# Kernel optimization log

Hardware: AMD Instinct MI355X
Metric: run time of the kernel (lower is better)

Reference implementation:

```python
import jax, jax.numpy as jnp
import numpy as np

N, E, G, P = 65536, 1048576, 512, 128   # nodes, edges, graphs, nodes per graph
K = 64                                   # sort-pool k (fixed in module)
NUM_CLASSES = 10
FEAT = 128


def _gcn_conv(x, W, b, src, dst):
    # PyG GCNConv: linear, add self-loops, symmetric-normalized aggregation, bias
    h = x @ W
    deg = jnp.ones((N,), x.dtype).at[dst].add(1.0)       # self-loop + in-degree
    dinv = jax.lax.rsqrt(deg)
    coef = (dinv[src] * dinv[dst])[:, None]
    agg = jax.ops.segment_sum(h[src] * coef, dst, num_segments=N)
    agg = agg + h * (dinv * dinv)[:, None]               # self-loop messages
    return agg + b


def setup_inputs() -> dict:
    key = jax.random.key(0)
    ks = jax.random.split(key, 12)
    x = jax.random.normal(ks[0], (N, FEAT), jnp.float32)
    src = jax.random.randint(ks[1], (E,), 0, N, dtype=jnp.int32)
    off = jax.random.randint(ks[2], (E,), 0, P, dtype=jnp.int32)
    dst = (src // P) * P + off                           # keep edges intra-graph
    edge_index = jnp.stack([src, dst])
    # balanced batch vector (implicit): node n belongs to graph n // P
    def lin(k, i, o):
        return jax.random.normal(k, (i, o), jnp.float32) / np.float32(np.sqrt(i))
    return {
        "x": x,
        "W1": lin(ks[3], FEAT, 128), "b1": jnp.zeros((128,), jnp.float32),
        "W2": lin(ks[4], 128, 64),   "b2": jnp.zeros((64,), jnp.float32),
        "W3": lin(ks[5], 64, 32),    "b3": jnp.zeros((32,), jnp.float32),
        "W4": lin(ks[6], 32, 32),    "b4": jnp.zeros((32,), jnp.float32),
        "W5": lin(ks[7], 256, 16).T, "b5": jnp.zeros((16,), jnp.float32),   # Conv1d(1,16,256,256)
        "W6": jax.random.normal(ks[8], (32, 16, 5), jnp.float32) * 0.1,      # Conv1d(16,32,5) OIH
        "b6": jnp.zeros((32,), jnp.float32),
        "Wf1": lin(ks[9], 896, 128), "bf1": jnp.zeros((128,), jnp.float32),
        "Wf2": lin(ks[10], 128, NUM_CLASSES), "bf2": jnp.zeros((NUM_CLASSES,), jnp.float32),
        "edge_index": edge_index,
    }


def reference(x, W1, b1, W2, b2, W3, b3, W4, b4, W5, b5, W6, b6,
              Wf1, bf1, Wf2, bf2, edge_index):
    src, dst = edge_index[0], edge_index[1]
    x1 = jnp.tanh(_gcn_conv(x, W1, b1, src, dst))
    x2 = jnp.tanh(_gcn_conv(x1, W2, b2, src, dst))
    x3 = jnp.tanh(_gcn_conv(x2, W3, b3, src, dst))
    x4 = jnp.tanh(_gcn_conv(x3, W4, b4, src, dst))
    h = jnp.concatenate([x1, x2, x3, x4], axis=-1)       # [N, 256]
    C = h.shape[-1]
    # global_sort_pool: balanced graphs of P nodes -> sort desc by last channel, take top-K
    hg = h.reshape(G, P, C)
    order = jnp.argsort(-hg[:, :, -1], axis=1)[:, :K]    # [G, K]
    pooled = jnp.take_along_axis(hg, order[:, :, None], axis=1)   # [G, K, C]
    # Conv1d(1, 16, 256, stride=256): kernel == stride == C, so per-node matmul
    z = jnp.einsum('gtj,cj->gct', pooled, W5) + b5[None, :, None]  # [G,16,64]
    z = jax.nn.relu(z)
    z = z.reshape(G, 16, -1, 2).max(axis=-1)                       # MaxPool1d(2,2) -> [G,16,32]
    z = jax.lax.conv_general_dilated(z, W6, (1,), 'VALID',
                                     dimension_numbers=('NCH', 'OIH', 'NCH'))
    z = jax.nn.relu(z + b6[None, :, None])                          # [G,32,28]
    z = z.reshape(G, -1)                                            # [G,896]
    out = jax.nn.relu(z @ Wf1 + bf1)
    # dropout is identity at eval time
    return jax.nn.log_softmax(out @ Wf2 + bf2, axis=-1)
```

## Files before the change

kernel.cpp:

```cpp
#include <hip/hip_runtime.h>

#define N_EDGES 1048576
#define N_GRAPH 512
#define MAXE    2560
#define CHUNK   2048
#define SBLK    (N_EDGES / CHUNK)

typedef __attribute__((ext_vector_type(4))) float floatx4;
typedef __attribute__((ext_vector_type(2))) float floatx2;
typedef __attribute__((ext_vector_type(4))) int intx4;

__global__ void scatter_kernel(const int* __restrict__ src, const int* __restrict__ dst,
                               unsigned* __restrict__ cstab, unsigned short* __restrict__ ebuf) {
    __shared__ unsigned short sbuf[CHUNK];
    __shared__ unsigned short sg[CHUNK];
    __shared__ unsigned lhist[512];
    __shared__ unsigned lscan[512];
    const int t = threadIdx.x;
    const int b = blockIdx.x;
    lhist[t] = 0; lhist[t + 256] = 0;
    __syncthreads();
    const intx4* s4 = (const intx4*)(src + b * CHUNK) + t * 2;
    const intx4* d4 = (const intx4*)(dst + b * CHUNK) + t * 2;
    unsigned short gg[8], pk[8], rr[8];
#pragma unroll
    for (int h = 0; h < 2; ++h) {
        intx4 sv = s4[h], dv = d4[h];
        int ss[4] = {sv.x, sv.y, sv.z, sv.w};
        int dd[4] = {dv.x, dv.y, dv.z, dv.w};
#pragma unroll
        for (int j = 0; j < 4; ++j) {
            unsigned g = ((unsigned)dd[j]) >> 7;
            gg[h * 4 + j] = (unsigned short)g;
            pk[h * 4 + j] = (unsigned short)((ss[j] & 127) | ((dd[j] & 127) << 8));
            rr[h * 4 + j] = (unsigned short)atomicAdd(&lhist[g], 1u);
        }
    }
    __syncthreads();
    unsigned a0 = lhist[t], a1 = lhist[t + 256];
    lscan[t] = a0; lscan[t + 256] = a1;
    __syncthreads();
    for (int d = 1; d < 512; d <<= 1) {
        unsigned v0 = (t >= d) ? lscan[t - d] : 0u;
        unsigned v1 = (t + 256 >= d) ? lscan[t + 256 - d] : 0u;
        __syncthreads();
        lscan[t] += v0; lscan[t + 256] += v1;
        __syncthreads();
    }
    lscan[t] -= a0; lscan[t + 256] -= a1;
    cstab[(size_t)t * SBLK + b]         = (a0 << 16) | lscan[t];
    cstab[(size_t)(t + 256) * SBLK + b] = (a1 << 16) | lscan[t + 256];
    __syncthreads();
#pragma unroll
    for (int j = 0; j < 8; ++j) {
        unsigned pos = lscan[gg[j]] + rr[j];
        sbuf[pos] = pk[j]; sg[pos] = gg[j];
    }
    __syncthreads();
    for (int i = t; i < CHUNK; i += 256)
        ebuf[(size_t)b * CHUNK + i] = sbuf[i];
    (void)sg;
}

template<int CIN, int COUT>
__device__ void gcn_layer(const float* Xin, float* Xio,
                          const float* __restrict__ W, const float* __restrict__ Bv,
                          const float* __restrict__ dinv, const int* __restrict__ offs,
                          const float* __restrict__ epack, int tid)
{
    constexpr int CL  = COUT / 4;
    constexpr int NPT = 128 / (1024 / CL);
    const int grp = tid / CL, cl = tid % CL;

    float acc[NPT][4];
#pragma unroll
    for (int ni = 0; ni < NPT; ++ni)
#pragma unroll
        for (int j = 0; j < 4; ++j) acc[ni][j] = 0.f;

    for (int k = 0; k < CIN; k += 4) {
        floatx4 xv[NPT];
#pragma unroll
        for (int ni = 0; ni < NPT; ++ni)
            xv[ni] = *(const floatx4*)(Xin + (grp * NPT + ni) * CIN + k);
#pragma unroll
        for (int i = 0; i < 4; ++i) {
            floatx4 wv = *(const floatx4*)(W + (k + i) * COUT + cl * 4);
#pragma unroll
            for (int ni = 0; ni < NPT; ++ni)
#pragma unroll
                for (int j = 0; j < 4; ++j)
                    acc[ni][j] += xv[ni][i] * wv[j];
        }
    }
    __syncthreads();
#pragma unroll
    for (int ni = 0; ni < NPT; ++ni) {
        floatx4 v; v[0] = acc[ni][0]; v[1] = acc[ni][1]; v[2] = acc[ni][2]; v[3] = acc[ni][3];
        *(floatx4*)(Xio + (grp * NPT + ni) * COUT + cl * 4) = v;
    }
    __syncthreads();

    floatx4 bv = *(const floatx4*)(Bv + cl * 4);
    float vout[NPT][4];
#pragma unroll
    for (int ni = 0; ni < NPT; ++ni) {
        int n = grp * NPT + ni;
        float a[4] = {0.f, 0.f, 0.f, 0.f};
        int o0 = offs[n], o1 = offs[n + 1];
        for (int p = o0; p < o1; ++p) {
            floatx2 e = *(const floatx2*)(epack + 2 * p);
            float cf = e[0];
            int s = (int)__float_as_uint(e[1]);
            floatx4 h = *(const floatx4*)(Xio + s * COUT + cl * 4);
#pragma unroll
            for (int j = 0; j < 4; ++j) a[j] += h[j] * cf;
        }
        float dn = dinv[n], dnn = dn * dn;
#pragma unroll
        for (int j = 0; j < 4; ++j)
            vout[ni][j] = tanhf(a[j] + acc[ni][j] * dnn + bv[j]);
    }
    __syncthreads();
#pragma unroll
    for (int ni = 0; ni < NPT; ++ni) {
        floatx4 v; v[0] = vout[ni][0]; v[1] = vout[ni][1]; v[2] = vout[ni][2]; v[3] = vout[ni][3];
        *(floatx4*)(Xio + (grp * NPT + ni) * COUT + cl * 4) = v;
    }
    __syncthreads();
}

__global__ __launch_bounds__(1024, 1) void mega_kernel(
    const float* __restrict__ x,
    const float* __restrict__ W1, const float* __restrict__ b1,
    const float* __restrict__ W2, const float* __restrict__ b2,
    const float* __restrict__ W3, const float* __restrict__ b3,
    const float* __restrict__ W4, const float* __restrict__ b4,
    const float* __restrict__ W5, const float* __restrict__ b5,
    const float* __restrict__ W6, const float* __restrict__ b6,
    const float* __restrict__ Wf1, const float* __restrict__ bf1,
    const float* __restrict__ Wf2, const float* __restrict__ bf2,
    const unsigned* __restrict__ cstab, const unsigned short* __restrict__ ebuf,
    float* __restrict__ out)
{
    __shared__ __align__(16) char pool[162048];
    int*   ldeg = (int*)(pool + 0);
    int*   offs = (int*)(pool + 512);
    float* dinv = (float*)(pool + 1040);
    float* key  = (float*)(pool + 1552);
    unsigned short* ord = (unsigned short*)(pool + 2064);
    float* epack = (float*)(pool + 2304);
    float* W5s   = (float*)(pool + 2304);
    float* X1   = (float*)(pool + 22784);
    float* X2   = (float*)(pool + 88320);
    float* X3   = (float*)(pool + 121088);
    float* X4   = (float*)(pool + 137472);
    float* SCR  = (float*)(pool + 153856);
    float* Zs   = SCR;
    float* ZMP  = SCR + 1024;
    float* Z896 = SCR;
    float* PART = SCR + 1024;
    float* FC1  = SCR + 896;
    float* LG   = SCR;

    const int g   = blockIdx.x;
    const int tid = threadIdx.x;

    int myc = 0;
    unsigned short ev[24];
    if (tid < SBLK) {
        unsigned cs = cstab[(size_t)g * SBLK + tid];
        int start = (int)(cs & 0xFFFFu);
        myc = (int)(cs >> 16);
        if (myc > 24) myc = 24;
        const unsigned short* run = ebuf + (size_t)tid * CHUNK + start;
#pragma unroll
        for (int w = 0; w < 24; ++w)
            ev[w] = (w < myc) ? run[w] : (unsigned short)0;
    }

    if (tid < 128) ldeg[tid] = 0;
    __syncthreads();
#pragma unroll
    for (int w = 0; w < 24; ++w)
        if (w < myc) atomicAdd(&ldeg[(ev[w] >> 8) & 127], 1);
    __syncthreads();
    if (tid < 64) {
        int v0 = ldeg[2 * tid], v1 = ldeg[2 * tid + 1];
        int s = v0 + v1;
        for (int d = 1; d < 64; d <<= 1) {
            int u = __shfl_up(s, d, 64);
            if (tid >= d) s += u;
        }
        int e1 = s - v1, e2 = s;
        offs[2 * tid + 1] = (e1 < MAXE) ? e1 : MAXE;
        offs[2 * tid + 2] = (e2 < MAXE) ? e2 : MAXE;
        if (tid == 0) offs[0] = 0;
    }
    if (tid >= 128 && tid < 256) {
        int n = tid - 128;
        dinv[n] = 1.0f / sqrtf((float)(1 + ldeg[n]));
    }
    __syncthreads();
    if (tid < 128) ldeg[tid] = offs[tid];
    __syncthreads();
#pragma unroll
    for (int w = 0; w < 24; ++w)
        if (w < myc) {
            int dn_ = (ev[w] >> 8) & 127, sn = ev[w] & 127;
            int p = atomicAdd(&ldeg[dn_], 1);
            if (p < MAXE) {
                floatx2 e; e[0] = dinv[sn] * dinv[dn_]; e[1] = __uint_as_float((unsigned)sn);
                *(floatx2*)(epack + 2 * p) = e;
            }
        }
    const float* xg = x + (size_t)g * 16384;
    for (int idx = tid; idx < 4096; idx += 1024)
        *(floatx4*)(X1 + idx * 4) = *(const floatx4*)(xg + idx * 4);
    __syncthreads();

    gcn_layer<128, 128>(X1, X1, W1, b1, dinv, offs, epack, tid);
    gcn_layer<128,  64>(X1, X2, W2, b2, dinv, offs, epack, tid);
    gcn_layer< 64,  32>(X2, X3, W3, b3, dinv, offs, epack, tid);
    gcn_layer< 32,  32>(X3, X4, W4, b4, dinv, offs, epack, tid);

    if (tid < 128) key[tid] = X4[tid * 32 + 31];
    if (tid < 64)  ord[tid] = (unsigned short)tid;
    __syncthreads();
    for (int idx = tid; idx < 4096; idx += 1024) W5s[idx] = W5[idx];
    __syncthreads();
    if (tid < 128) {
        float myk = key[tid];
        int r = 0;
        for (int j = 0; j < 128; ++j) {
            float kj = key[j];
            r += (kj > myk) || (kj == myk && j < tid);
        }
        if (r < 64) ord[r] = (unsigned short)tid;
    }
    __syncthreads();

    {
        int q = tid >> 6, t = tid & 63;
        int node = ord[t] & 127;
        float z0 = b5[q];
        const float* w5a = W5s + q * 256;
        floatx4 zv = {0.f, 0.f, 0.f, 0.f};
        for (int jj = 0; jj < 32; ++jj) {
            int j = (jj + t) & 31;
            floatx4 pv = *(const floatx4*)(X1 + node * 128 + j * 4);
            floatx4 wv = *(const floatx4*)(w5a + j * 4);
#pragma unroll
            for (int u = 0; u < 4; ++u) zv[u] += pv[u] * wv[u];
        }
        for (int jj = 0; jj < 16; ++jj) {
            int j = (jj + t) & 15;
            floatx4 pv = *(const floatx4*)(X2 + node * 64 + j * 4);
            floatx4 wv = *(const floatx4*)(w5a + 128 + j * 4);
#pragma unroll
            for (int u = 0; u < 4; ++u) zv[u] += pv[u] * wv[u];
        }
        for (int jj = 0; jj < 8; ++jj) {
            int j = (jj + t) & 7;
            floatx4 pv = *(const floatx4*)(X3 + node * 32 + j * 4);
            floatx4 wv = *(const floatx4*)(w5a + 192 + j * 4);
#pragma unroll
            for (int u = 0; u < 4; ++u) zv[u] += pv[u] * wv[u];
        }
        for (int jj = 0; jj < 8; ++jj) {
            int j = (jj + t) & 7;
            floatx4 pv = *(const floatx4*)(X4 + node * 32 + j * 4);
            floatx4 wv = *(const floatx4*)(w5a + 224 + j * 4);
#pragma unroll
            for (int u = 0; u < 4; ++u) zv[u] += pv[u] * wv[u];
        }
        z0 += zv[0] + zv[1] + zv[2] + zv[3];
        Zs[q * 64 + t] = fmaxf(z0, 0.f);
    }
    __syncthreads();
    if (tid < 512) {
        int c = tid >> 5, p = tid & 31;
        ZMP[c * 32 + p] = fmaxf(Zs[c * 64 + 2 * p], Zs[c * 64 + 2 * p + 1]);
    }
    __syncthreads();
    for (int idx = tid; idx < 2560; idx += 1024) W5s[idx] = W6[idx];
    __syncthreads();
    if (tid < 896) {
        int oc = tid / 28, p = tid % 28;
        float s = b6[oc];
#pragma unroll
        for (int i = 0; i < 16; ++i) {
            const float* wrow = W5s + (oc * 16 + i) * 5;
#pragma unroll
            for (int k = 0; k < 5; ++k)
                s += ZMP[i * 32 + p + k] * wrow[k];
        }
        Z896[tid] = fmaxf(s, 0.f);
    }
    __syncthreads();
    {
        int f = tid & 127, q = tid >> 7;
        float s = 0.f;
        for (int i = q * 112; i < (q + 1) * 112; ++i)
            s += Z896[i] * Wf1[i * 128 + f];
        PART[q * 128 + f] = s;
    }
    __syncthreads();
    if (tid < 128) {
        float s = bf1[tid];
#pragma unroll
        for (int q = 0; q < 8; ++q) s += PART[q * 128 + tid];
        FC1[tid] = fmaxf(s, 0.f);
    }
    __syncthreads();
    if (tid < 10) {
        float s = bf2[tid];
        for (int i = 0; i < 128; ++i) s += FC1[i] * Wf2[i * 10 + tid];
        LG[tid] = s;
    }
    __syncthreads();
    if (tid == 0) {
        float mx = LG[0];
        for (int i = 1; i < 10; ++i) mx = fmaxf(mx, LG[i]);
        float se = 0.f;
        for (int i = 0; i < 10; ++i) se += expf(LG[i] - mx);
        LG[16] = mx + logf(se);
    }
    __syncthreads();
    if (tid < 10)
        out[g * 10 + tid] = LG[tid] - LG[16];
}

extern "C" void kernel_launch(void* const* d_in, const int* in_sizes, int n_in,
                              void* d_out, int out_size, void* d_ws, size_t ws_size,
                              hipStream_t stream) {
    (void)in_sizes; (void)n_in; (void)out_size; (void)ws_size;
    const float* x   = (const float*)d_in[0];
    const float* W1  = (const float*)d_in[1];
    const float* b1  = (const float*)d_in[2];
    const float* W2  = (const float*)d_in[3];
    const float* b2  = (const float*)d_in[4];
    const float* W3  = (const float*)d_in[5];
    const float* b3  = (const float*)d_in[6];
    const float* W4  = (const float*)d_in[7];
    const float* b4  = (const float*)d_in[8];
    const float* W5  = (const float*)d_in[9];
    const float* b5  = (const float*)d_in[10];
    const float* W6  = (const float*)d_in[11];
    const float* b6  = (const float*)d_in[12];
    const float* Wf1 = (const float*)d_in[13];
    const float* bf1 = (const float*)d_in[14];
    const float* Wf2 = (const float*)d_in[15];
    const float* bf2 = (const float*)d_in[16];
    const int* ei  = (const int*)d_in[17];
    const int* src = ei;
    const int* dst = ei + N_EDGES;

    char* ws = (char*)d_ws;
    unsigned short* ebuf = (unsigned short*)(ws);
    unsigned*       cstab = (unsigned*)(ws + 2097152);

    scatter_kernel<<<SBLK, 256, 0, stream>>>(src, dst, cstab, ebuf);
    mega_kernel<<<N_GRAPH, 1024, 0, stream>>>(x, W1, b1, W2, b2, W3, b3, W4, b4,
                                              W5, b5, W6, b6, Wf1, bf1, Wf2, bf2,
                                              cstab, ebuf, (float*)d_out);
}
```

Before: 279.1 us.

## Compute Conv1d projection for all nodes per layer, unroll edge aggregation by two

Applies the W5 projection to every node's features right after each GCN layer, accumulating a 16-channel per-node result, so the post-sort stage only gathers and pools precomputed values. This lets the shared-memory layout reuse the X1 region for later scratch space. The edge aggregation loop is also unrolled by two to overlap the indirect loads. In exchange it does twice the projection work (128 nodes instead of the 64 kept after sorting) and adds a barrier-free pass after each layer, reading W5 from global memory.

```diff
diff --git a/kernel.cpp b/kernel.cpp
--- a/kernel.cpp
+++ b/kernel.cpp
@@ -108,13 +108,23 @@
         int n = grp * NPT + ni;
         float a[4] = {0.f, 0.f, 0.f, 0.f};
         int o0 = offs[n], o1 = offs[n + 1];
-        for (int p = o0; p < o1; ++p) {
+        int p = o0;
+        for (; p + 1 < o1; p += 2) {
+            floatx2 e0 = *(const floatx2*)(epack + 2 * p);
+            floatx2 e1 = *(const floatx2*)(epack + 2 * p + 2);
+            int s0 = (int)__float_as_uint(e0[1]);
+            int s1 = (int)__float_as_uint(e1[1]);
+            floatx4 h0 = *(const floatx4*)(Xio + s0 * COUT + cl * 4);
+            floatx4 h1 = *(const floatx4*)(Xio + s1 * COUT + cl * 4);
+#pragma unroll
+            for (int j = 0; j < 4; ++j) a[j] += h0[j] * e0[0] + h1[j] * e1[0];
+        }
+        if (p < o1) {
             floatx2 e = *(const floatx2*)(epack + 2 * p);
-            float cf = e[0];
             int s = (int)__float_as_uint(e[1]);
             floatx4 h = *(const floatx4*)(Xio + s * COUT + cl * 4);
 #pragma unroll
-            for (int j = 0; j < 4; ++j) a[j] += h[j] * cf;
+            for (int j = 0; j < 4; ++j) a[j] += h[j] * e[0];
         }
         float dn = dinv[n], dnn = dn * dn;
 #pragma unroll
@@ -128,6 +138,30 @@
         *(floatx4*)(Xio + (grp * NPT + ni) * COUT + cl * 4) = v;
     }
     __syncthreads();
+}
+
+template<int LEN, int OFF, bool INIT>
+__device__ void yacc(const float* __restrict__ Xl, float* __restrict__ Y,
+                     const float* __restrict__ W5, int tid)
+{
+    const int c = tid & 15;
+    const int n0 = tid >> 4;
+#pragma unroll
+    for (int h = 0; h < 2; ++h) {
+        int n = n0 + h * 64;
+        const float* xr = Xl + n * LEN;
+        const float* wr = W5 + c * 256 + OFF;
+        floatx4 s4v = {0.f, 0.f, 0.f, 0.f};
+        for (int j = 0; j < LEN; j += 4) {
+            floatx4 xv = *(const floatx4*)(xr + j);
+            floatx4 wv = *(const floatx4*)(wr + j);
+#pragma unroll
+            for (int u = 0; u < 4; ++u) s4v[u] += xv[u] * wv[u];
+        }
+        float s = s4v[0] + s4v[1] + s4v[2] + s4v[3];
+        if constexpr (INIT) Y[n * 16 + c] = s;
+        else                Y[n * 16 + c] += s;
+    }
 }
 
 __global__ __launch_bounds__(1024, 1) void mega_kernel(
@@ -150,18 +184,17 @@
     float* key  = (float*)(pool + 1552);
     unsigned short* ord = (unsigned short*)(pool + 2064);
     float* epack = (float*)(pool + 2304);
-    float* W5s   = (float*)(pool + 2304);
     float* X1   = (float*)(pool + 22784);
     float* X2   = (float*)(pool + 88320);
     float* X3   = (float*)(pool + 121088);
     float* X4   = (float*)(pool + 137472);
-    float* SCR  = (float*)(pool + 153856);
-    float* Zs   = SCR;
-    float* ZMP  = SCR + 1024;
-    float* Z896 = SCR;
-    float* PART = SCR + 1024;
-    float* FC1  = SCR + 896;
-    float* LG   = SCR;
+    float* Y    = (float*)(pool + 153856);
+    float* ZMP  = (float*)(pool + 22784);
+    float* W6s  = (float*)(pool + 22784 + 2048);
+    float* Z896 = (float*)(pool + 22784 + 12288);
+    float* PART = (float*)(pool + 22784 + 15872);
+    float* FC1  = (float*)(pool + 22784 + 19968);
+    float* LG   = (float*)(pool + 22784 + 20480);
 
     const int g   = blockIdx.x;
     const int tid = threadIdx.x;
@@ -220,14 +253,17 @@
     __syncthreads();
 
     gcn_layer<128, 128>(X1, X1, W1, b1, dinv, offs, epack, tid);
+    yacc<128,   0, true >(X1, Y, W5, tid);
     gcn_layer<128,  64>(X1, X2, W2, b2, dinv, offs, epack, tid);
+    yacc< 64, 128, false>(X2, Y, W5, tid);
     gcn_layer< 64,  32>(X2, X3, W3, b3, dinv, offs, epack, tid);
+    yacc< 32, 192, false>(X3, Y, W5, tid);
     gcn_layer< 32,  32>(X3, X4, W4, b4, dinv, offs, epack, tid);
+    yacc< 32, 224, false>(X4, Y, W5, tid);
 
     if (tid < 128) key[tid] = X4[tid * 32 + 31];
-    if (tid < 64)  ord[tid] = (unsigned short)tid;
-    __syncthreads();
-    for (int idx = tid; idx < 4096; idx += 1024) W5s[idx] = W5[idx];
+    if (tid >= 896 && tid < 960) ord[tid - 896] = (unsigned short)(tid - 896);
+    for (int idx = tid; idx < 2560; idx += 1024) W6s[idx] = W6[idx];
     __syncthreads();
     if (tid < 128) {
         float myk = key[tid];
@@ -240,57 +276,21 @@
     }
     __syncthreads();
 
-    {
-        int q = tid >> 6, t = tid & 63;
-        int node = ord[t] & 127;
-        float z0 = b5[q];
-        const float* w5a = W5s + q * 256;
-        floatx4 zv = {0.f, 0.f, 0.f, 0.f};
-        for (int jj = 0; jj < 32; ++jj) {
-            int j = (jj + t) & 31;
-            floatx4 pv = *(const floatx4*)(X1 + node * 128 + j * 4);
-            floatx4 wv = *(const floatx4*)(w5a + j * 4);
-#pragma unroll
-            for (int u = 0; u < 4; ++u) zv[u] += pv[u] * wv[u];
-        }
-        for (int jj = 0; jj < 16; ++jj) {
-            int j = (jj + t) & 15;
-            floatx4 pv = *(const floatx4*)(X2 + node * 64 + j * 4);
-            floatx4 wv = *(const floatx4*)(w5a + 128 + j * 4);
-#pragma unroll
-            for (int u = 0; u < 4; ++u) zv[u] += pv[u] * wv[u];
-        }
-        for (int jj = 0; jj < 8; ++jj) {
-            int j = (jj + t) & 7;
-            floatx4 pv = *(const floatx4*)(X3 + node * 32 + j * 4);
-            floatx4 wv = *(const floatx4*)(w5a + 192 + j * 4);
-#pragma unroll
-            for (int u = 0; u < 4; ++u) zv[u] += pv[u] * wv[u];
-        }
-        for (int jj = 0; jj < 8; ++jj) {
-            int j = (jj + t) & 7;
-            floatx4 pv = *(const floatx4*)(X4 + node * 32 + j * 4);
-            floatx4 wv = *(const floatx4*)(w5a + 224 + j * 4);
-#pragma unroll
-            for (int u = 0; u < 4; ++u) zv[u] += pv[u] * wv[u];
-        }
-        z0 += zv[0] + zv[1] + zv[2] + zv[3];
-        Zs[q * 64 + t] = fmaxf(z0, 0.f);
-    }
-    __syncthreads();
     if (tid < 512) {
-        int c = tid >> 5, p = tid & 31;
-        ZMP[c * 32 + p] = fmaxf(Zs[c * 64 + 2 * p], Zs[c * 64 + 2 * p + 1]);
-    }
-    __syncthreads();
-    for (int idx = tid; idx < 2560; idx += 1024) W5s[idx] = W6[idx];
+        int c = tid & 15, pp = tid >> 4;
+        int n0 = ord[2 * pp] & 127, n1 = ord[2 * pp + 1] & 127;
+        float b = b5[c];
+        float z0 = fmaxf(b + Y[n0 * 16 + c], 0.f);
+        float z1 = fmaxf(b + Y[n1 * 16 + c], 0.f);
+        ZMP[c * 32 + pp] = fmaxf(z0, z1);
+    }
     __syncthreads();
     if (tid < 896) {
         int oc = tid / 28, p = tid % 28;
         float s = b6[oc];
 #pragma unroll
         for (int i = 0; i < 16; ++i) {
-            const float* wrow = W5s + (oc * 16 + i) * 5;
+            const float* wrow = W6s + (oc * 16 + i) * 5;
 #pragma unroll
             for (int k = 0; k < 5; ++k)
                 s += ZMP[i * 32 + p + k] * wrow[k];
```

Measured after the change: 327.6 us. +17.4%, slower.
